# Kernel tuning notes

Hardware: AMD Instinct MI355X
Metric: run time of the kernel (lower is better)

The kernel has to match this reference:

```python
import jax, jax.numpy as jnp
import numpy as np

# ContextualAttention config (matches init_kwargs)
KS, STRIDE, DIL, FUSE_K, SCALE = 3, 1, 1, 3, 10.0
B, C, H, W = 2, 128, 64, 64
L = H * W  # number of background patches (SAME padding, stride 1)


def _same_pad(x, k, s):
    # TF-style SAME padding, identical to the repo's same_padding helper
    _, _, h, w = x.shape
    oh, ow = -(-h // s), -(-w // s)
    ph = max(0, (oh - 1) * s + k - h)
    pw = max(0, (ow - 1) * s + k - w)
    return jnp.pad(x, ((0, 0), (0, 0), (ph // 2, ph - ph // 2), (pw // 2, pw - pw // 2)))


def _patches(x, k, s):
    # extract_image_patches: SAME pad + unfold -> [N, L, C*k*k], (c, kh, kw) ordering
    xp = _same_pad(x, k, s)
    n, c, hp, wp = xp.shape
    oh, ow = (hp - k) // s + 1, (wp - k) // s + 1
    cols = jnp.stack(
        [xp[:, :, i:i + (oh - 1) * s + 1:s, j:j + (ow - 1) * s + 1:s]
         for i in range(k) for j in range(k)], axis=2)  # [N, C, k*k, oh, ow]
    return cols.reshape(n, c * k * k, oh * ow).transpose(0, 2, 1)


def _fuse(scores):
    # diagonal fuse-smoothing: conv the [L_b, L_f] score matrix with eye(k), twice
    # (second pass on the transposed spatial layout), exactly as in the torch code
    bn = scores.shape[0]
    eye = jnp.eye(FUSE_K, dtype=scores.dtype)[None, None]  # [1,1,k,k]
    conv = lambda v: jax.lax.conv_general_dilated(
        v, eye, (1, 1), [(1, 1), (1, 1)],
        dimension_numbers=('NCHW', 'OIHW', 'NCHW'))
    y = conv(scores.reshape(bn, 1, L, L))
    y = y.reshape(bn, H, W, H, W).transpose(0, 2, 1, 4, 3).reshape(bn, 1, L, L)
    y = conv(y)
    y = y.reshape(bn, W, H, W, H).transpose(0, 2, 1, 4, 3)  # back to [b,H,W,H,W]
    return y.reshape(bn, L, H, W)


def setup_inputs() -> dict:
    key = jax.random.key(0)
    kf, kb, km = jax.random.split(key, 3)
    f = jax.random.normal(kf, (B, C, H, W), jnp.float32)
    b = jax.random.normal(kb, (B, C, H, W), jnp.float32)
    mask = (jax.random.uniform(km, (1, 1, H, W)) < 0.05).astype(jnp.float32)
    return {"f": f, "b": b, "mask": mask}


def reference(f, b, mask):
    kernel = 2 * DIL  # raw patch size for aggregation (=2)
    # raw background patches used by the transposed-conv aggregation
    raw_w = _patches(b, kernel, DIL * STRIDE).reshape(B, L, C, kernel, kernel)
    # DIL == 1 => F.interpolate(scale=1.0, nearest) is identity on f/b/mask
    w = _patches(b, KS, STRIDE)      # [B, L, C*9] matching patches
    fp = _patches(f, KS, 1)          # [B, Lf, C*9] foreground patches (SAME pad)
    m = _patches(mask, KS, STRIDE)[0]                    # [L, 9]
    mm = (jnp.mean(m, axis=1) == 0.0).astype(f.dtype)    # [L] 1 = patch usable

    # per-patch L2 normalization (clamped at 1e-4), conv-as-similarity == patch GEMM
    wn = w / jnp.maximum(jnp.sqrt(jnp.sum(w * w, axis=2, keepdims=True)), 1e-4)
    scores = jnp.einsum('bkd,bqd->bkq', wn, fp).reshape(B, L, H, W)
    scores = _fuse(scores)

    mmb = mm[None, :, None, None]
    attn = jax.nn.softmax(scores * mmb * SCALE, axis=1) * mmb  # softmax over L

    # conv_transpose2d(attn, raw_w, stride=1, padding=1) == VALID corr with flipped,
    # IO-swapped 2x2 kernel (k-1-p = 0 padding); per-sample weights -> vmap
    def agg(a, rw):  # a: [L,H,W], rw: [L,C,2,2]
        rhs = jnp.flip(rw, axis=(2, 3)).transpose(1, 0, 2, 3)  # [C, L, 2, 2] OIHW
        return jax.lax.conv_general_dilated(
            a[None], rhs, (1, 1), [(0, 0), (0, 0)],
            dimension_numbers=('NCHW', 'OIHW', 'NCHW'))[0]

    y = jax.vmap(agg)(attn, raw_w) / 4.0       # [B, C, H-1, W-1]
    y = jnp.pad(y, ((0, 0), (0, 0), (0, 1), (0, 1)))  # output_padding = DIL % 2 = 1
    return y
```

## Files before the change

kernel.cpp:

```cpp
#include <hip/hip_runtime.h>

#define L 4096
#define HH 64
#define CC 128
#define BB 2

typedef _Float16 f16;
typedef _Float16 f16x8 __attribute__((ext_vector_type(8)));
typedef float f32x4 __attribute__((ext_vector_type(4)));

__device__ __forceinline__ void gl_lds16(const f16* g, f16* l) {
  __builtin_amdgcn_global_load_lds(
      (const __attribute__((address_space(1))) void*)g,
      (__attribute__((address_space(3))) void*)l, 16, 0, 0);
}

__device__ __forceinline__ int sigma_(int j) { return ((j & 63) << 6) | (j >> 6); }

__device__ float fuse9(const f16* __restrict__ Sb, int k, int j) {
  float acc = 0.f;
  int cK = sigma_(k), cQ = sigma_(j);
#pragma unroll
  for (int u = -1; u <= 1; ++u) {
    int a = cK + u, bq = cQ + u;
    if ((unsigned)a < L && (unsigned)bq < L) {
      int r = sigma_(a), c = sigma_(bq);
#pragma unroll
      for (int t = -1; t <= 1; ++t) {
        int rr = r + t, cc = c + t;
        if ((unsigned)rr < L && (unsigned)cc < L) acc += (float)Sb[(size_t)rr * L + cc];
      }
    }
  }
  return acc;
}

__global__ __launch_bounds__(256) void k_repack(
    const float* __restrict__ b, const float* __restrict__ f,
    f16* __restrict__ bT, f16* __restrict__ fT, f16* __restrict__ zp) {
  __shared__ float tile[128][65];
  int u0 = blockIdx.x * 64;
  int z = blockIdx.y;
  int batch = z >> 1;
  const float* src = ((z & 1) ? f : b) + (size_t)batch * CC * L;
  f16* dst = ((z & 1) ? fT : bT) + (size_t)batch * L * CC;
  int tid = threadIdx.x;
  if (blockIdx.x == 0 && z == 0 && tid < 32) zp[tid] = (f16)0.f;
#pragma unroll
  for (int i = 0; i < 32; ++i) {
    int idx = i * 256 + tid;
    int c = idx >> 6, ux = idx & 63;
    tile[c][ux] = src[(size_t)c * L + u0 + ux];
  }
  __syncthreads();
#pragma unroll
  for (int j = 0; j < 4; ++j) {
    int t2 = j * 256 + tid;
    int u = t2 >> 4, ch = t2 & 15;
    f16x8 v;
#pragma unroll
    for (int e = 0; e < 8; ++e) v[e] = (f16)tile[ch * 8 + e][u];
    *(f16x8*)(dst + (size_t)(u0 + u) * CC + ch * 8) = v;
  }
}

__global__ __launch_bounds__(256) void k_ssq(const float* __restrict__ b, float* __restrict__ ssq) {
  int u = blockIdx.x * 256 + threadIdx.x;
  int batch = blockIdx.y;
  const float* bp = b + (size_t)batch * CC * L + u;
  float s = 0.f;
#pragma unroll 4
  for (int c = 0; c < CC; ++c) { float v = bp[(size_t)c * L]; s += v * v; }
  ssq[batch * L + u] = s;
}

__global__ void k_norm(const float* __restrict__ ssq, float* __restrict__ inv_n) {
  int gi = blockIdx.x * 256 + threadIdx.x;
  if (gi >= BB * L) return;
  int batch = gi >> 12, k = gi & (L - 1);
  int ky = k >> 6, kx = k & 63;
  float s = 0.f;
#pragma unroll
  for (int dy = -1; dy <= 1; ++dy)
#pragma unroll
    for (int dx = -1; dx <= 1; ++dx) {
      if ((unsigned)(ky + dy) < 64 && (unsigned)(kx + dx) < 64)
        s += ssq[batch * L + k + dy * 64 + dx];
    }
  inv_n[gi] = 1.f / fmaxf(sqrtf(s), 1e-4f);
}

__global__ __launch_bounds__(256) void k_prep_bm(const float* __restrict__ b, f16* __restrict__ bm) {
  int idx = blockIdx.x * 256 + threadIdx.x;
  int e8 = idx * 8;
  int k0 = e8 & (L - 1);
  int c = (e8 >> 12) & (CC - 1);
  int bt = e8 >> 19;
  int batch = bt & 1;
  int tap = bt >> 1;
  int di = 1 - (tap >> 1), dj = 1 - (tap & 1);
  int ky = k0 >> 6, kx0 = k0 & 63;
  const float* src = b + ((size_t)batch * CC + c) * L + k0 + di * 64 + dj;
  bool rowok = (ky + di) < 64;
  f16x8 v;
#pragma unroll
  for (int e = 0; e < 8; ++e) {
    float x = (rowok && (kx0 + e + dj) < 64) ? src[e] : 0.f;
    v[e] = (f16)x;
  }
  *(f16x8*)(bm + (size_t)e8) = v;
}

__global__ void k_prep_mm(const float* __restrict__ mask, float* __restrict__ mmv) {
  int k = blockIdx.x * 256 + threadIdx.x;
  if (k >= L) return;
  int ky = k >> 6, kx = k & 63;
  float s = 0.f;
  for (int i = 0; i < 3; ++i)
    for (int j = 0; j < 3; ++j) {
      int yy = ky + i - 1, xx = kx + j - 1;
      if (yy >= 0 && yy < 64 && xx >= 0 && xx < 64) s += mask[yy * 64 + xx];
    }
  mmv[k] = (s == 0.f) ? 1.f : 0.f;
}

__global__ __launch_bounds__(256) void k_gemm_scores(
    const f16* __restrict__ bT, const f16* __restrict__ fT,
    const float* __restrict__ inv_n, const f16* __restrict__ zp,
    f16* __restrict__ S) {
  __shared__ f16 As[128 * 64];
  __shared__ f16 Bs[128 * 64];
  int qt = blockIdx.x, kt = blockIdx.y, batch = blockIdx.z;
  int tid = threadIdx.x, wid = tid >> 6, lane = tid & 63;
  int wr = wid >> 1, wc = wid & 1;
  const f16* A0 = bT + (size_t)batch * L * CC;
  const f16* B0 = fT + (size_t)batch * L * CC;
  f32x4 acc[4][4] = {};
  int rA = wr * 64 + (lane & 15);
  int rB = wc * 64 + (lane & 15);

  const f16* baseA_[4]; const f16* baseB_[4];
  f16* ldsA_[4]; f16* ldsB_[4];
  unsigned mA_[4], mB_[4];
#pragma unroll
  for (int i = 0; i < 4; ++i) {
    int chunk = (i * 4 + wid) * 64 + lane;
    int row = chunk >> 3;
    int lg = (lane & 7) ^ (row & 7);
    int k = kt * 128 + row;
    int q = qt * 128 + row;
    baseA_[i] = A0 + (size_t)k * CC + lg * 8;
    baseB_[i] = B0 + (size_t)q * CC + lg * 8;
    ldsA_[i] = As + chunk * 8;
    ldsB_[i] = Bs + chunk * 8;
    int ky = k >> 6, kx = k & 63, qy = q >> 6, qx = q & 63;
    unsigned ma = 0, mb = 0;
#pragma unroll
    for (int rr = 0; rr < 9; ++rr) {
      int dy = rr / 3 - 1, dx = rr - (rr / 3) * 3 - 1;
      if ((unsigned)(ky + dy) < 64u && (unsigned)(kx + dx) < 64u) ma |= 1u << rr;
      if ((unsigned)(qy + dy) < 64u && (unsigned)(qx + dx) < 64u) mb |= 1u << rr;
    }
    mA_[i] = ma; mB_[i] = mb;
  }

#pragma unroll 1
  for (int t = 0; t < 18; ++t) {
    int rr = t >> 1, half = t & 1;
    int dy = rr / 3 - 1, dx = rr - (rr / 3) * 3 - 1;
    int doff = (dy * 64 + dx) * CC + half * 64;
    __syncthreads();
#pragma unroll
    for (int i = 0; i < 4; ++i) {
      gl_lds16(((mA_[i] >> rr) & 1u) ? (baseA_[i] + doff) : zp, ldsA_[i]);
      gl_lds16(((mB_[i] >> rr) & 1u) ? (baseB_[i] + doff) : zp, ldsB_[i]);
    }
    __syncthreads();
#pragma unroll
    for (int h2 = 0; h2 < 2; ++h2) {
      int cb = h2 * 4 + (lane >> 4);
      f16x8 af[4], bf[4];
#pragma unroll
      for (int m = 0; m < 4; ++m) {
        int row = rA + m * 16;
        af[m] = *(const f16x8*)(As + row * 64 + ((cb ^ (row & 7)) * 8));
      }
#pragma unroll
      for (int n = 0; n < 4; ++n) {
        int row = rB + n * 16;
        bf[n] = *(const f16x8*)(Bs + row * 64 + ((cb ^ (row & 7)) * 8));
      }
#pragma unroll
      for (int m = 0; m < 4; ++m)
#pragma unroll
        for (int n = 0; n < 4; ++n)
          acc[m][n] = __builtin_amdgcn_mfma_f32_16x16x32_f16(af[m], bf[n], acc[m][n], 0, 0, 0);
    }
  }
  f16* Srow = S + (size_t)batch * L * L;
  int kbase = kt * 128 + wr * 64 + (lane >> 4) * 4;
  int qbase = qt * 128 + wc * 64 + (lane & 15);
#pragma unroll
  for (int m = 0; m < 4; ++m) {
    f32x4 invv = *(const f32x4*)(inv_n + (size_t)batch * L + kbase + m * 16);
#pragma unroll
    for (int r = 0; r < 4; ++r) {
      f16* dst = Srow + (size_t)(kbase + m * 16 + r) * L + qbase;
#pragma unroll
      for (int n = 0; n < 4; ++n) dst[n * 16] = (f16)(acc[m][n][r] * invv[r]);
    }
  }
}

__global__ __launch_bounds__(256) void k_fuse_stats(
    const f16* __restrict__ S, const float* __restrict__ mmv,
    float* __restrict__ T3, float* __restrict__ pm, float* __restrict__ pl) {
  int tid = threadIdx.x;
  if (tid >= 247) return;
  int jc = blockIdx.x, kc = blockIdx.y, batch = blockIdx.z;
  int g = jc * 247 + tid;
  int q0 = 72 + g * 8;
  const f16* Sb = S + (size_t)batch * L * L;
  float* Tb = T3 + (size_t)batch * L * L;
  float m8[8], l8[8];
#pragma unroll
  for (int e = 0; e < 8; ++e) { m8[e] = -3.0e38f; l8[e] = 0.f; }
  int cnt = 0;
  int k0 = kc * 16;
  for (int kk = 0; kk < 16; ++kk) {
    int k = k0 + kk;
    if (mmv[k] == 0.f) { ++cnt; continue; }
    float acc[8] = {0.f, 0.f, 0.f, 0.f, 0.f, 0.f, 0.f, 0.f};
    int cK = sigma_(k);
#pragma unroll
    for (int u = -1; u <= 1; ++u) {
      int a = cK + u;
      if ((unsigned)a >= L) continue;
      int r = sigma_(a);
      const f16* cb = Sb + (size_t)r * L + (q0 + 64 * u);
      {
        f16x8 v = *(const f16x8*)cb;
#pragma unroll
        for (int e = 0; e < 8; ++e) acc[e] += (float)v[e];
      }
      if (r >= 1) {
        const f16* rm = cb - L;
        f16x8 v = *(const f16x8*)rm;
        acc[0] += (float)rm[-1];
#pragma unroll
        for (int e = 1; e < 8; ++e) acc[e] += (float)v[e - 1];
      }
      if (r <= L - 2) {
        const f16* rp = cb + L;
        f16x8 v = *(const f16x8*)rp;
#pragma unroll
        for (int e = 0; e < 7; ++e) acc[e] += (float)v[e + 1];
        acc[7] += (float)rp[8];
      }
    }
#pragma unroll
    for (int e = 0; e < 8; ++e) acc[e] *= 10.f;
    float* trow = Tb + (size_t)k * L + q0;
    *(f32x4*)trow = *(f32x4*)&acc[0];
    *(f32x4*)(trow + 4) = *(f32x4*)&acc[4];
#pragma unroll
    for (int e = 0; e < 8; ++e) {
      float nm = fmaxf(m8[e], acc[e]);
      l8[e] = l8[e] * __expf(m8[e] - nm) + __expf(acc[e] - nm);
      m8[e] = nm;
    }
  }
  float fc = (float)cnt;
  float om[8], ol[8];
#pragma unroll
  for (int e = 0; e < 8; ++e) {
    float nm = fmaxf(m8[e], 0.f);
    ol[e] = l8[e] * __expf(m8[e] - nm) + fc * __expf(-nm);
    om[e] = nm;
  }
  float* pmp = pm + (size_t)kc * (BB * L) + (size_t)batch * L + q0;
  float* plp = pl + (size_t)kc * (BB * L) + (size_t)batch * L + q0;
  *(f32x4*)pmp = *(f32x4*)&om[0]; *(f32x4*)(pmp + 4) = *(f32x4*)&om[4];
  *(f32x4*)plp = *(f32x4*)&ol[0]; *(f32x4*)(plp + 4) = *(f32x4*)&ol[4];
}

__global__ __launch_bounds__(256) void k_fuse_stats_edge(
    const f16* __restrict__ S, const float* __restrict__ mmv,
    float* __restrict__ T3, float* __restrict__ pm, float* __restrict__ pl) {
  int tid = threadIdx.x;
  if (tid >= 144) return;
  int q = (tid < 72) ? tid : (4024 + tid - 72);
  int kc = blockIdx.x, batch = blockIdx.y;
  const f16* Sb = S + (size_t)batch * L * L;
  float* Tb = T3 + (size_t)batch * L * L;
  float m = -3.0e38f, l = 0.f;
  int cnt = 0;
  int k0 = kc * 16;
  for (int kk = 0; kk < 16; ++kk) {
    int k = k0 + kk;
    if (mmv[k] == 0.f) { ++cnt; continue; }
    float logit = 10.f * fuse9(Sb, k, q);
    Tb[(size_t)k * L + q] = logit;
    float nm = fmaxf(m, logit);
    l = l * __expf(m - nm) + __expf(logit - nm);
    m = nm;
  }
  float nm = fmaxf(m, 0.f);
  l = l * __expf(m - nm) + (float)cnt * __expf(-nm);
  pm[(size_t)kc * (BB * L) + (size_t)batch * L + q] = nm;
  pl[(size_t)kc * (BB * L) + (size_t)batch * L + q] = l;
}

__global__ void k_softmax_reduce(const float* __restrict__ pm, const float* __restrict__ pl,
                                 float* __restrict__ Mq, float* __restrict__ invLq) {
  int qi = blockIdx.x * 256 + threadIdx.x;
  if (qi >= BB * L) return;
  float M = -3.0e38f;
  for (int i = 0; i < 256; ++i) M = fmaxf(M, pm[(size_t)i * (BB * L) + qi]);
  float Ls = 0.f;
  for (int i = 0; i < 256; ++i) Ls += pl[(size_t)i * (BB * L) + qi] * __expf(pm[(size_t)i * (BB * L) + qi] - M);
  Mq[qi] = M;
  invLq[qi] = 1.f / Ls;
}

__global__ __launch_bounds__(512) void k_agg(
    const float* __restrict__ T3, const float* __restrict__ mmv,
    const float* __restrict__ Mq, const float* __restrict__ invLq,
    const f16* __restrict__ bm, float* __restrict__ part) {
  __shared__ f16 Asm[512 * 32];
  __shared__ f16 Bt[136 * 40];
  int pt = blockIdx.x, ks = blockIdx.y, batch = blockIdx.z;
  int p0 = pt * 64;
  int tid = threadIdx.x, wid = tid >> 6, lane = tid & 63;
  int wr = wid >> 1, wc = wid & 1;
  const float* Tb = T3 + (size_t)batch * L * L;
  const float* mq0 = Mq + (size_t)batch * L;
  const float* il0 = invLq + (size_t)batch * L;
  f32x4 acc[2][2] = {};
  int kend = ks * 1024 + 1024;
  for (int k0 = ks * 1024; k0 < kend; k0 += 32) {
    __syncthreads();
#pragma unroll
    for (int i = 0; i < 4; ++i) {
      int R = wid * 64 + i * 16 + (lane >> 2);
      int tap = R >> 7, c = R & 127;
      int chl = (lane & 3) ^ ((R >> 1) & 3);
      const f16* g = bm + (((size_t)(tap * 2 + batch) * CC + c) * L) + k0 + chl * 8;
      gl_lds16(g, Asm + R * 32 + (lane & 3) * 8);
    }
    for (int tau = tid; tau < 544; tau += 512) {
      int kk = tau / 17, ch = tau - kk * 17;
      int k = k0 + kk;
      int pbase = p0 + ch * 8;
      f16 v[8];
      if (mmv[k] != 0.f) {
        const float* trow = Tb + (size_t)k * L + pbase;
        if (pbase + 7 < L) {
          f32x4 t0 = *(const f32x4*)trow;
          f32x4 t1 = *(const f32x4*)(trow + 4);
          f32x4 m0 = *(const f32x4*)(mq0 + pbase);
          f32x4 m1 = *(const f32x4*)(mq0 + pbase + 4);
          f32x4 i0 = *(const f32x4*)(il0 + pbase);
          f32x4 i1 = *(const f32x4*)(il0 + pbase + 4);
#pragma unroll
          for (int e = 0; e < 4; ++e) v[e] = (f16)(__expf(t0[e] - m0[e]) * i0[e]);
#pragma unroll
          for (int e = 0; e < 4; ++e) v[4 + e] = (f16)(__expf(t1[e] - m1[e]) * i1[e]);
        } else {
#pragma unroll
          for (int e = 0; e < 8; ++e) {
            int q = pbase + e;
            v[e] = (q < L) ? (f16)(__expf(trow[e] - mq0[q]) * il0[q]) : (f16)0.f;
          }
        }
      } else {
#pragma unroll
        for (int e = 0; e < 8; ++e) v[e] = (f16)0.f;
      }
#pragma unroll
      for (int e = 0; e < 8; ++e) {
        int pp = ch * 8 + e;
        Bt[pp * 40 + (((kk >> 3) ^ ((pp >> 3) & 3)) * 8) + (kk & 7)] = v[e];
      }
    }
    __syncthreads();
#pragma unroll
    for (int tap = 0; tap < 4; ++tap) {
      int dlt = (tap >> 1) * 64 + (tap & 1);
      f16x8 af[2], bf[2];
#pragma unroll
      for (int m = 0; m < 2; ++m) {
        int R = tap * 128 + wr * 32 + m * 16 + (lane & 15);
        int ph = (lane >> 4) ^ ((R >> 1) & 3);
        af[m] = *(const f16x8*)(Asm + R * 32 + ph * 8);
      }
#pragma unroll
      for (int n = 0; n < 2; ++n) {
        int pp = wc * 32 + n * 16 + (lane & 15) + dlt;
        int ph = (lane >> 4) ^ ((pp >> 3) & 3);
        bf[n] = *(const f16x8*)(Bt + pp * 40 + ph * 8);
      }
#pragma unroll
      for (int m = 0; m < 2; ++m)
#pragma unroll
        for (int n = 0; n < 2; ++n)
          acc[m][n] = __builtin_amdgcn_mfma_f32_16x16x32_f16(af[m], bf[n], acc[m][n], 0, 0, 0);
    }
  }
  int cb = wr * 32 + (lane >> 4) * 4;
  int pb = p0 + wc * 32 + (lane & 15);
#pragma unroll
  for (int m = 0; m < 2; ++m)
#pragma unroll
    for (int n = 0; n < 2; ++n)
#pragma unroll
      for (int r = 0; r < 4; ++r) {
        int c = cb + m * 16 + r;
        int p = pb + n * 16;
        part[(((size_t)ks * 2 + batch) * CC + c) * L + p] = acc[m][n][r];
      }
}

__global__ __launch_bounds__(256) void k_agg_reduce(const float* __restrict__ part, float* __restrict__ out) {
  int idx = (blockIdx.x * 256 + threadIdx.x) * 4;
  f32x4 s = {0.f, 0.f, 0.f, 0.f};
#pragma unroll
  for (int ks = 0; ks < 4; ++ks) {
    f32x4 v = *(const f32x4*)(part + (size_t)ks * (2 * CC * L) + idx);
#pragma unroll
    for (int e = 0; e < 4; ++e) s[e] += v[e];
  }
  int p = idx & (L - 1);
  int u = p >> 6, vv = p & 63;
  f32x4 o;
#pragma unroll
  for (int e = 0; e < 4; ++e) o[e] = (u < 63 && (vv + e) < 63) ? s[e] * 0.25f : 0.f;
  *(f32x4*)(out + idx) = o;
}

extern "C" void kernel_launch(void* const* d_in, const int* in_sizes, int n_in,
                              void* d_out, int out_size, void* d_ws, size_t ws_size,
                              hipStream_t stream) {
  const float* f = (const float*)d_in[0];
  const float* b = (const float*)d_in[1];
  const float* mask = (const float*)d_in[2];
  float* out = (float*)d_out;
  char* ws = (char*)d_ws;

  float* T3  = (float*)(ws + 0);
  f16* S     = (f16*)(ws + 134217728);
  f16* bm    = (f16*)(ws + 201326592);
  float* part= (float*)(ws + 209715200);
  float* pm  = (float*)(ws + 226492416);
  float* pl  = (float*)(ws + 234881024);
  float* mmv = (float*)(ws + 243269632);
  float* Mq  = (float*)(ws + 243286016);
  float* iLq = (float*)(ws + 243318784);
  f16* bT    = (f16*)(ws + 243351552);
  f16* fT    = (f16*)(ws + 245448704);
  float* ssq = (float*)(ws + 247545856);
  float* invn= (float*)(ws + 247578624);
  f16* zp    = (f16*)(ws + 247611392);

  k_repack<<<dim3(64, 4), dim3(256), 0, stream>>>(b, f, bT, fT, zp);
  k_ssq<<<dim3(16, 2), dim3(256), 0, stream>>>(b, ssq);
  k_norm<<<dim3(32), dim3(256), 0, stream>>>(ssq, invn);
  k_prep_bm<<<dim3(2048), dim3(256), 0, stream>>>(b, bm);
  k_prep_mm<<<dim3(16), dim3(256), 0, stream>>>(mask, mmv);
  k_gemm_scores<<<dim3(32, 32, 2), dim3(256), 0, stream>>>(bT, fT, invn, zp, S);
  k_fuse_stats<<<dim3(2, 256, 2), dim3(256), 0, stream>>>(S, mmv, T3, pm, pl);
  k_fuse_stats_edge<<<dim3(256, 2), dim3(256), 0, stream>>>(S, mmv, T3, pm, pl);
  k_softmax_reduce<<<dim3(32), dim3(256), 0, stream>>>(pm, pl, Mq, iLq);
  k_agg<<<dim3(64, 4, 2), dim3(512), 0, stream>>>(T3, mmv, Mq, iLq, bm, part);
  k_agg_reduce<<<dim3(1024), dim3(256), 0, stream>>>(part, out);
}
```

Before: 374.4 us.

## Double-buffer score GEMM LDS loads and parallelize softmax reduce across partitions

The score GEMM now keeps two LDS buffers per operand and issues the global-to-LDS loads for the next K step before running MFMAs on the current one. This removes one barrier per iteration and is meant to overlap memory latency with compute, at the cost of doubling LDS use to 64KB, which may reduce occupancy. The softmax reduce kernel now splits the 256 partials across four waves with an online max/sum merge through shared memory, launching four times as many blocks to give more parallelism on a small kernel.

```diff
diff --git a/kernel.cpp b/kernel.cpp
--- a/kernel.cpp
+++ b/kernel.cpp
@@ -128,8 +128,8 @@
     const f16* __restrict__ bT, const f16* __restrict__ fT,
     const float* __restrict__ inv_n, const f16* __restrict__ zp,
     f16* __restrict__ S) {
-  __shared__ f16 As[128 * 64];
-  __shared__ f16 Bs[128 * 64];
+  __shared__ f16 As[2][128 * 64];
+  __shared__ f16 Bs[2][128 * 64];
   int qt = blockIdx.x, kt = blockIdx.y, batch = blockIdx.z;
   int tid = threadIdx.x, wid = tid >> 6, lane = tid & 63;
   int wr = wid >> 1, wc = wid & 1;
@@ -140,7 +140,7 @@
   int rB = wc * 64 + (lane & 15);
 
   const f16* baseA_[4]; const f16* baseB_[4];
-  f16* ldsA_[4]; f16* ldsB_[4];
+  int offL_[4];
   unsigned mA_[4], mB_[4];
 #pragma unroll
   for (int i = 0; i < 4; ++i) {
@@ -151,8 +151,7 @@
     int q = qt * 128 + row;
     baseA_[i] = A0 + (size_t)k * CC + lg * 8;
     baseB_[i] = B0 + (size_t)q * CC + lg * 8;
-    ldsA_[i] = As + chunk * 8;
-    ldsB_[i] = Bs + chunk * 8;
+    offL_[i] = chunk * 8;
     int ky = k >> 6, kx = k & 63, qy = q >> 6, qx = q & 63;
     unsigned ma = 0, mb = 0;
 #pragma unroll
@@ -164,18 +163,28 @@
     mA_[i] = ma; mB_[i] = mb;
   }
 
+#define STAGE_T(tt, bsel)                                                     \
+  do {                                                                        \
+    int rr_ = (tt) >> 1, half_ = (tt) & 1;                                    \
+    int dy_ = rr_ / 3 - 1, dx_ = rr_ - (rr_ / 3) * 3 - 1;                     \
+    int doff_ = (dy_ * 64 + dx_) * CC + half_ * 64;                           \
+    _Pragma("unroll")                                                         \
+    for (int i = 0; i < 4; ++i) {                                             \
+      gl_lds16(((mA_[i] >> rr_) & 1u) ? (baseA_[i] + doff_) : zp,             \
+               &As[bsel][0] + offL_[i]);                                      \
+      gl_lds16(((mB_[i] >> rr_) & 1u) ? (baseB_[i] + doff_) : zp,             \
+               &Bs[bsel][0] + offL_[i]);                                      \
+    }                                                                         \
+  } while (0)
+
+  STAGE_T(0, 0);
+  int cur = 0;
 #pragma unroll 1
   for (int t = 0; t < 18; ++t) {
-    int rr = t >> 1, half = t & 1;
-    int dy = rr / 3 - 1, dx = rr - (rr / 3) * 3 - 1;
-    int doff = (dy * 64 + dx) * CC + half * 64;
     __syncthreads();
-#pragma unroll
-    for (int i = 0; i < 4; ++i) {
-      gl_lds16(((mA_[i] >> rr) & 1u) ? (baseA_[i] + doff) : zp, ldsA_[i]);
-      gl_lds16(((mB_[i] >> rr) & 1u) ? (baseB_[i] + doff) : zp, ldsB_[i]);
-    }
-    __syncthreads();
+    if (t < 17) STAGE_T(t + 1, cur ^ 1);
+    const f16* Ab = &As[cur][0];
+    const f16* Bb = &Bs[cur][0];
 #pragma unroll
     for (int h2 = 0; h2 < 2; ++h2) {
       int cb = h2 * 4 + (lane >> 4);
@@ -183,12 +192,12 @@
 #pragma unroll
       for (int m = 0; m < 4; ++m) {
         int row = rA + m * 16;
-        af[m] = *(const f16x8*)(As + row * 64 + ((cb ^ (row & 7)) * 8));
+        af[m] = *(const f16x8*)(Ab + row * 64 + ((cb ^ (row & 7)) * 8));
       }
 #pragma unroll
       for (int n = 0; n < 4; ++n) {
         int row = rB + n * 16;
-        bf[n] = *(const f16x8*)(Bs + row * 64 + ((cb ^ (row & 7)) * 8));
+        bf[n] = *(const f16x8*)(Bb + row * 64 + ((cb ^ (row & 7)) * 8));
       }
 #pragma unroll
       for (int m = 0; m < 4; ++m)
@@ -196,7 +205,10 @@
         for (int n = 0; n < 4; ++n)
           acc[m][n] = __builtin_amdgcn_mfma_f32_16x16x32_f16(af[m], bf[n], acc[m][n], 0, 0, 0);
     }
-  }
+    cur ^= 1;
+  }
+#undef STAGE_T
+
   f16* Srow = S + (size_t)batch * L * L;
   int kbase = kt * 128 + wr * 64 + (lane >> 4) * 4;
   int qbase = qt * 128 + wc * 64 + (lane & 15);
@@ -311,16 +323,35 @@
   pl[(size_t)kc * (BB * L) + (size_t)batch * L + q] = l;
 }
 
-__global__ void k_softmax_reduce(const float* __restrict__ pm, const float* __restrict__ pl,
-                                 float* __restrict__ Mq, float* __restrict__ invLq) {
-  int qi = blockIdx.x * 256 + threadIdx.x;
-  if (qi >= BB * L) return;
-  float M = -3.0e38f;
-  for (int i = 0; i < 256; ++i) M = fmaxf(M, pm[(size_t)i * (BB * L) + qi]);
-  float Ls = 0.f;
-  for (int i = 0; i < 256; ++i) Ls += pl[(size_t)i * (BB * L) + qi] * __expf(pm[(size_t)i * (BB * L) + qi] - M);
-  Mq[qi] = M;
-  invLq[qi] = 1.f / Ls;
+__global__ __launch_bounds__(256) void k_softmax_reduce(
+    const float* __restrict__ pm, const float* __restrict__ pl,
+    float* __restrict__ Mq, float* __restrict__ invLq) {
+  __shared__ float sm[4][64], sl[4][64];
+  int tid = threadIdx.x;
+  int ql = tid & 63, part = tid >> 6;
+  int qi = blockIdx.x * 64 + ql;
+  float m = -3.0e38f, l = 0.f;
+  int i0 = part * 64;
+#pragma unroll 4
+  for (int i = i0; i < i0 + 64; ++i) {
+    float pmv = pm[(size_t)i * (BB * L) + qi];
+    float plv = pl[(size_t)i * (BB * L) + qi];
+    float nm = fmaxf(m, pmv);
+    l = l * __expf(m - nm) + plv * __expf(pmv - nm);
+    m = nm;
+  }
+  sm[part][ql] = m; sl[part][ql] = l;
+  __syncthreads();
+  if (part == 0) {
+    float M = sm[0][ql];
+#pragma unroll
+    for (int p = 1; p < 4; ++p) M = fmaxf(M, sm[p][ql]);
+    float Ls = 0.f;
+#pragma unroll
+    for (int p = 0; p < 4; ++p) Ls += sl[p][ql] * __expf(sm[p][ql] - M);
+    Mq[qi] = M;
+    invLq[qi] = 1.f / Ls;
+  }
 }
 
 __global__ __launch_bounds__(512) void k_agg(
@@ -470,7 +501,7 @@
   k_gemm_scores<<<dim3(32, 32, 2), dim3(256), 0, stream>>>(bT, fT, invn, zp, S);
   k_fuse_stats<<<dim3(2, 256, 2), dim3(256), 0, stream>>>(S, mmv, T3, pm, pl);
   k_fuse_stats_edge<<<dim3(256, 2), dim3(256), 0, stream>>>(S, mmv, T3, pm, pl);
-  k_softmax_reduce<<<dim3(32), dim3(256), 0, stream>>>(pm, pl, Mq, iLq);
+  k_softmax_reduce<<<dim3(128), dim3(256), 0, stream>>>(pm, pl, Mq, iLq);
   k_agg<<<dim3(64, 4, 2), dim3(512), 0, stream>>>(T3, mmv, Mq, iLq, bm, part);
   k_agg_reduce<<<dim3(1024), dim3(256), 0, stream>>>(part, out);
 }
```

Measured after the change: 321.0 us. 1.17x faster.
